# Kernel optimization log

Measured on AMD Instinct MI355X. Metric: run time of the kernel, lower is better.

Reference implementation:

```python
import jax, jax.numpy as jnp
import numpy as np

# Config mirrors init_kwargs
D_IN, D_OUT, HEADS, SEQ, BATCH = 1024, 64, 16, 2048, 2


def setup_inputs() -> dict:
    key = jax.random.key(0)
    kx, kq, kk, kv = jax.random.split(key, 4)
    scale = 1.0 / np.sqrt(D_IN)
    x = jax.random.normal(kx, (BATCH, SEQ, D_IN), dtype=jnp.float32)
    # Stacked per-head projection weights, [H, d_in, d_out] (qkv_bias=False)
    Wq = jax.random.normal(kq, (HEADS, D_IN, D_OUT), dtype=jnp.float32) * scale
    Wk = jax.random.normal(kk, (HEADS, D_IN, D_OUT), dtype=jnp.float32) * scale
    Wv = jax.random.normal(kv, (HEADS, D_IN, D_OUT), dtype=jnp.float32) * scale
    return {"x": x, "Wq": Wq, "Wk": Wk, "Wv": Wv}


def reference(x, Wq, Wk, Wv):
    # x: [B, S, d_in]; W*: [H, d_in, d_out]
    q = jnp.einsum("bsd,hde->bhse", x, Wq)
    k = jnp.einsum("bsd,hde->bhse", x, Wk)
    v = jnp.einsum("bsd,hde->bhse", x, Wv)
    scores = jnp.einsum("bhse,bhte->bhst", q, k) / jnp.sqrt(
        jnp.asarray(D_OUT, dtype=q.dtype)
    )
    S = x.shape[1]
    causal = jnp.tril(jnp.ones((S, S), dtype=bool))  # [S, S]
    scores = jnp.where(causal[None, None], scores, -jnp.inf)
    attn = jax.nn.softmax(scores, axis=-1)  # dropout=0.0 (eval)
    ctx = jnp.einsum("bhst,bhte->bhse", attn, v)  # [B, H, S, d_out]
    # concat heads on last dim -> [B, S, H*d_out]
    B, H, S2, E = ctx.shape
    return jnp.transpose(ctx, (0, 2, 1, 3)).reshape(B, S2, H * E)
```

## Files before the change

### kernel.cpp

```cpp
#include <hip/hip_runtime.h>
#include <hip/hip_bf16.h>
#include <math.h>

#define BATCH 2
#define SEQ   2048
#define DIN   1024
#define HEADS 16
#define EDIM  64

#define NX   (BATCH*SEQ*DIN)
#define NW   (3*HEADS*DIN*EDIM)
#define NQKV (BATCH*HEADS*SEQ*EDIM)

#define QSCALE 0.18033688011112042f

typedef __attribute__((ext_vector_type(8))) short short8;
typedef __attribute__((ext_vector_type(4))) float f32x4;

static __device__ __forceinline__ ushort f2bf(float f) {
    __hip_bfloat16 h = __float2bfloat16(f);
    return *reinterpret_cast<ushort*>(&h);
}

__global__ __launch_bounds__(256) void prep(
    const float* __restrict__ x, const float* __restrict__ Wq,
    const float* __restrict__ Wk, const float* __restrict__ Wv,
    ushort* __restrict__ xb, ushort* __restrict__ wt)
{
    const int t = threadIdx.x;
    if (blockIdx.x < 1024) {
        const int v0 = blockIdx.x * 256 + t;
#pragma unroll
        for (int i = 0; i < 4; ++i) {
            int i4 = (v0 + i * 262144) * 4;
            float4 f = *(const float4*)(x + i4);
            ushort4 o;
            o.x = f2bf(f.x); o.y = f2bf(f.y); o.z = f2bf(f.z); o.w = f2bf(f.w);
            *(ushort4*)(xb + i4) = o;
        }
    } else {
        const int bid = blockIdx.x - 1024;
        const int dt  = bid & 15;
        const int h   = (bid >> 4) & 15;
        const int mat = bid >> 8;

        const float* W = (mat == 0) ? Wq : (mat == 1) ? Wk : Wv;
        const float* src = W + ((size_t)h * DIN + dt * 64) * EDIM;
        ushort* dst = wt + ((size_t)(mat * HEADS + h) * EDIM) * DIN + dt * 64;

        __shared__ ushort T[64][68];
#pragma unroll
        for (int i = 0; i < 16; ++i) {
            int v = t + i * 256;
            int d = v >> 6, e = v & 63;
            T[d][e] = f2bf(src[(size_t)d * EDIM + e]);
        }
        __syncthreads();
#pragma unroll
        for (int i = 0; i < 4; ++i) {
            int v = t + i * 256;
            int e = v >> 4, d4 = (v & 15) << 2;
            ushort4 ov;
            ov.x = T[d4 + 0][e]; ov.y = T[d4 + 1][e];
            ov.z = T[d4 + 2][e]; ov.w = T[d4 + 3][e];
            *(ushort4*)&dst[(size_t)e * DIN + d4] = ov;
        }
    }
}

__global__ __launch_bounds__(256) void qkv_gemm(
    const ushort* __restrict__ xb, const ushort* __restrict__ wt,
    ushort* __restrict__ qkv)
{
    const int bid = blockIdx.x;
    const int xcd = bid & 7;
    const int idx = bid >> 3;
    const int mt  = (xcd >> 1) * 8 + idx / 12;
    const int nt  = (xcd & 1) * 12 + idx % 12;
    const int m0 = mt * 128, n0 = nt * 128;
    const int b  = mt >> 4;

    __shared__ ushort Xs[128][72];
    __shared__ ushort Ws[128][72];

    const int t    = threadIdx.x;
    const int lane = t & 63;
    const int w    = t >> 6;
    const int wr   = w >> 1, wc = w & 1;
    const int fr   = lane & 15;
    const int fk   = (lane >> 4) * 8;
    const int rg   = (lane >> 4) * 4;

    const ushort* xbase = xb + (size_t)m0 * DIN;
    const ushort* wbase = wt + (size_t)n0 * DIN;

    ushort4 xr[8], wr2[8];
#pragma unroll
    for (int i = 0; i < 8; ++i) {
        int v = t + i * 256;
        xr[i]  = *(const ushort4*)&xbase[(size_t)(v >> 4) * DIN + ((v & 15) << 2)];
        wr2[i] = *(const ushort4*)&wbase[(size_t)(v >> 4) * DIN + ((v & 15) << 2)];
    }

    f32x4 acc[4][4];
#pragma unroll
    for (int i = 0; i < 4; ++i)
#pragma unroll
        for (int j = 0; j < 4; ++j) acc[i][j] = (f32x4)0.f;

    for (int kt = 0; kt < DIN / 64; ++kt) {
        __syncthreads();
#pragma unroll
        for (int i = 0; i < 8; ++i) {
            int v = t + i * 256;
            *(ushort4*)&Xs[v >> 4][(v & 15) << 2] = xr[i];
            *(ushort4*)&Ws[v >> 4][(v & 15) << 2] = wr2[i];
        }
        __syncthreads();
        if (kt + 1 < DIN / 64) {
            const int k0 = (kt + 1) * 64;
#pragma unroll
            for (int i = 0; i < 8; ++i) {
                int v = t + i * 256;
                xr[i]  = *(const ushort4*)&xbase[(size_t)(v >> 4) * DIN + k0 + ((v & 15) << 2)];
                wr2[i] = *(const ushort4*)&wbase[(size_t)(v >> 4) * DIN + k0 + ((v & 15) << 2)];
            }
        }
        short8 a[4][2], bfr[4][2];
#pragma unroll
        for (int rb = 0; rb < 4; ++rb)
#pragma unroll
            for (int kk = 0; kk < 2; ++kk) {
                a[rb][kk]   = *(const short8*)&Xs[wr * 64 + rb * 16 + fr][kk * 32 + fk];
                bfr[rb][kk] = *(const short8*)&Ws[wc * 64 + rb * 16 + fr][kk * 32 + fk];
            }
#pragma unroll
        for (int kk = 0; kk < 2; ++kk)
#pragma unroll
            for (int rb = 0; rb < 4; ++rb)
#pragma unroll
                for (int cf = 0; cf < 4; ++cf)
                    acc[rb][cf] = __builtin_amdgcn_mfma_f32_16x16x32_bf16(a[rb][kk], bfr[cf][kk], acc[rb][cf], 0, 0, 0);
    }

    const int hg  = nt * 2 + wc;
    const int mat = hg >> 4;
    const int h   = hg & 15;
    const int s0  = (m0 & 2047) + wr * 64;
    if (mat < 2) {
        const float sc = (mat == 0) ? QSCALE : 1.0f;
        ushort* dst = qkv + (size_t)mat * NQKV
                    + ((size_t)((b * HEADS + h) * SEQ) + s0) * EDIM;
#pragma unroll
        for (int rb = 0; rb < 4; ++rb)
#pragma unroll
            for (int cf = 0; cf < 4; ++cf)
#pragma unroll
                for (int i = 0; i < 4; ++i)
                    dst[(size_t)(rb * 16 + rg + i) * EDIM + cf * 16 + fr] = f2bf(acc[rb][cf][i] * sc);
    } else {
        ushort* vtb = qkv + (size_t)2 * NQKV + ((size_t)(b * HEADS + h) * EDIM) * SEQ;
#pragma unroll
        for (int rb = 0; rb < 4; ++rb)
#pragma unroll
            for (int cf = 0; cf < 4; ++cf) {
                ushort4 ov;
                ov.x = f2bf(acc[rb][cf][0]); ov.y = f2bf(acc[rb][cf][1]);
                ov.z = f2bf(acc[rb][cf][2]); ov.w = f2bf(acc[rb][cf][3]);
                *(ushort4*)&vtb[(size_t)(cf * 16 + fr) * SEQ + s0 + rb * 16 + rg] = ov;
            }
    }
}

__global__ __launch_bounds__(512) void flash_mfma(
    const ushort* __restrict__ q, const ushort* __restrict__ k,
    const ushort* __restrict__ vt, float* __restrict__ out)
{
    const int bid = blockIdx.x;
    const int it  = 15 - (bid >> 5);
    const int bh  = bid & 31;
    const int b   = bh >> 4;
    const int h   = bh & 15;
    const int KT  = 2 * it + 2;

    const ushort* Qb  = q  + ((size_t)((b * HEADS + h) * SEQ) + it * 128) * EDIM;
    const ushort* Kb  = k  + ((size_t)((b * HEADS + h) * SEQ)) * EDIM;
    const ushort* Vtb = vt + ((size_t)((b * HEADS + h) * EDIM)) * SEQ;

    __shared__ ushort Ks_[2][64][72];
    __shared__ ushort Vs_[2][64][72];
    __shared__ ushort Ps_[8][16][72];

    const int t    = threadIdx.x;
    const int lane = t & 63;
    const int w    = t >> 6;
    const int fr   = lane & 15;
    const int fk   = (lane >> 4) * 8;
    const int rg   = (lane >> 4) * 4;

    const int srow = t >> 3;
    const int scol = (t & 7) * 8;

    const int wrow0 = it * 128 + w * 16;
    const int lastT = wrow0 >> 6;
    const int qrow  = wrow0 + fr;

    short8 qf[2];
#pragma unroll
    for (int kk = 0; kk < 2; ++kk)
        qf[kk] = *(const short8*)&Qb[(size_t)(w * 16 + fr) * EDIM + kk * 32 + fk];

    f32x4 o_[4];
#pragma unroll
    for (int cf = 0; cf < 4; ++cf) o_[cf] = (f32x4)0.f;
    float lpart = 0.f;

    uint4 krv = *(const uint4*)&Kb[(size_t)srow * EDIM + scol];
    uint4 vrv = *(const uint4*)&Vtb[(size_t)srow * SEQ + scol];
    *(uint4*)&Ks_[0][srow][scol] = krv;
    *(uint4*)&Vs_[0][srow][scol] = vrv;
    __syncthreads();

    for (int kt = 0; kt < KT; ++kt) {
        const int cur = kt & 1;

        if (kt + 1 < KT) {
            krv = *(const uint4*)&Kb[(size_t)((kt + 1) * 64 + srow) * EDIM + scol];
            vrv = *(const uint4*)&Vtb[(size_t)srow * SEQ + (kt + 1) * 64 + scol];
        }

        if (kt <= lastT) {
            f32x4 s[4];
#pragma unroll
            for (int cf = 0; cf < 4; ++cf) s[cf] = (f32x4)0.f;
#pragma unroll
            for (int cf = 0; cf < 4; ++cf)
#pragma unroll
                for (int kk = 0; kk < 2; ++kk) {
                    short8 kf = *(const short8*)&Ks_[cur][cf * 16 + fr][kk * 32 + fk];
                    s[cf] = __builtin_amdgcn_mfma_f32_16x16x32_bf16(kf, qf[kk], s[cf], 0, 0, 0);
                }

            const bool dm = (kt == lastT);
            if (dm) {
#pragma unroll
                for (int cf = 0; cf < 4; ++cf)
#pragma unroll
                    for (int i = 0; i < 4; ++i) {
                        int kpos = kt * 64 + cf * 16 + rg + i;
                        if (kpos > qrow) s[cf][i] = -1e30f;
                    }
            }

            float ls = 0.f;
#pragma unroll
            for (int cf = 0; cf < 4; ++cf) {
                float p0 = __builtin_amdgcn_exp2f(s[cf][0]);
                float p1 = __builtin_amdgcn_exp2f(s[cf][1]);
                float p2 = __builtin_amdgcn_exp2f(s[cf][2]);
                float p3 = __builtin_amdgcn_exp2f(s[cf][3]);
                ls += (p0 + p1) + (p2 + p3);
                uint2 pk;
                pk.x = (uint)f2bf(p0) | ((uint)f2bf(p1) << 16);
                pk.y = (uint)f2bf(p2) | ((uint)f2bf(p3) << 16);
                *(uint2*)&Ps_[w][fr][cf * 16 + rg] = pk;
            }
            lpart += ls;

            short8 pf[2];
#pragma unroll
            for (int kb = 0; kb < 2; ++kb)
                pf[kb] = *(const short8*)&Ps_[w][fr][kb * 32 + fk];
#pragma unroll
            for (int cf = 0; cf < 4; ++cf)
#pragma unroll
                for (int kb = 0; kb < 2; ++kb) {
                    short8 vf = *(const short8*)&Vs_[cur][cf * 16 + fr][kb * 32 + fk];
                    o_[cf] = __builtin_amdgcn_mfma_f32_16x16x32_bf16(vf, pf[kb], o_[cf], 0, 0, 0);
                }
        }

        if (kt + 1 < KT) {
            const int nxt = cur ^ 1;
            *(uint4*)&Ks_[nxt][srow][scol] = krv;
            *(uint4*)&Vs_[nxt][srow][scol] = vrv;
            __syncthreads();
        }
    }

    float ls = lpart;
    ls += __shfl_xor(ls, 16);
    ls += __shfl_xor(ls, 32);
    const float inv = 1.f / ls;

    float* rowp = out + ((size_t)(b * SEQ + qrow)) * (HEADS * EDIM) + h * EDIM;
#pragma unroll
    for (int cf = 0; cf < 4; ++cf) {
        f32x4 ov = o_[cf] * inv;
        *(f32x4*)&rowp[cf * 16 + rg] = ov;
    }
}

extern "C" void kernel_launch(void* const* d_in, const int* in_sizes, int n_in,
                              void* d_out, int out_size, void* d_ws, size_t ws_size,
                              hipStream_t stream) {
    const float* x  = (const float*)d_in[0];
    const float* Wq = (const float*)d_in[1];
    const float* Wk = (const float*)d_in[2];
    const float* Wv = (const float*)d_in[3];
    float* out = (float*)d_out;

    ushort* xb  = (ushort*)d_ws;
    ushort* wt  = xb + NX;
    ushort* qkv = wt + NW;

    prep<<<1792, 256, 0, stream>>>(x, Wq, Wk, Wv, xb, wt);
    qkv_gemm<<<768, 256, 0, stream>>>(xb, wt, qkv);
    flash_mfma<<<BATCH * HEADS * (SEQ / 128), 512, 0, stream>>>(
        qkv, qkv + NQKV, qkv + (size_t)2 * NQKV, out);
}
```

Baseline: 95.37 us.

## Give each flash wave two query row blocks and widen GEMM tile loads

The attention kernel drops from 8 waves of 16 query rows each to 4 waves of 32 rows each. Each K and V fragment read from shared memory is now reused for two MFMA row blocks, which halves LDS fragment traffic per unit of math but raises register pressure and cuts the number of waves per block. The QKV GEMM switches its global and LDS tile loads from 8-byte to 16-byte vectors, issuing half as many load and store instructions. The coarser causal work split means a wave may compute one extra partially masked tile.

```diff
diff --git a/kernel.cpp b/kernel.cpp
--- a/kernel.cpp
+++ b/kernel.cpp
@@ -94,12 +94,12 @@
     const ushort* xbase = xb + (size_t)m0 * DIN;
     const ushort* wbase = wt + (size_t)n0 * DIN;
 
-    ushort4 xr[8], wr2[8];
-#pragma unroll
-    for (int i = 0; i < 8; ++i) {
-        int v = t + i * 256;
-        xr[i]  = *(const ushort4*)&xbase[(size_t)(v >> 4) * DIN + ((v & 15) << 2)];
-        wr2[i] = *(const ushort4*)&wbase[(size_t)(v >> 4) * DIN + ((v & 15) << 2)];
+    uint4 xr[4], wr2[4];
+#pragma unroll
+    for (int i = 0; i < 4; ++i) {
+        int c = t + i * 256;
+        xr[i]  = *(const uint4*)&xbase[(size_t)(c >> 3) * DIN + ((c & 7) << 3)];
+        wr2[i] = *(const uint4*)&wbase[(size_t)(c >> 3) * DIN + ((c & 7) << 3)];
     }
 
     f32x4 acc[4][4];
@@ -111,19 +111,19 @@
     for (int kt = 0; kt < DIN / 64; ++kt) {
         __syncthreads();
 #pragma unroll
-        for (int i = 0; i < 8; ++i) {
-            int v = t + i * 256;
-            *(ushort4*)&Xs[v >> 4][(v & 15) << 2] = xr[i];
-            *(ushort4*)&Ws[v >> 4][(v & 15) << 2] = wr2[i];
+        for (int i = 0; i < 4; ++i) {
+            int c = t + i * 256;
+            *(uint4*)&Xs[c >> 3][(c & 7) << 3] = xr[i];
+            *(uint4*)&Ws[c >> 3][(c & 7) << 3] = wr2[i];
         }
         __syncthreads();
         if (kt + 1 < DIN / 64) {
             const int k0 = (kt + 1) * 64;
 #pragma unroll
-            for (int i = 0; i < 8; ++i) {
-                int v = t + i * 256;
-                xr[i]  = *(const ushort4*)&xbase[(size_t)(v >> 4) * DIN + k0 + ((v & 15) << 2)];
-                wr2[i] = *(const ushort4*)&wbase[(size_t)(v >> 4) * DIN + k0 + ((v & 15) << 2)];
+            for (int i = 0; i < 4; ++i) {
+                int c = t + i * 256;
+                xr[i]  = *(const uint4*)&xbase[(size_t)(c >> 3) * DIN + k0 + ((c & 7) << 3)];
+                wr2[i] = *(const uint4*)&wbase[(size_t)(c >> 3) * DIN + k0 + ((c & 7) << 3)];
             }
         }
         short8 a[4][2], bfr[4][2];
@@ -172,7 +172,7 @@
     }
 }
 
-__global__ __launch_bounds__(512) void flash_mfma(
+__global__ __launch_bounds__(256) void flash_mfma(
     const ushort* __restrict__ q, const ushort* __restrict__ k,
     const ushort* __restrict__ vt, float* __restrict__ out)
 {
@@ -189,7 +189,7 @@
 
     __shared__ ushort Ks_[2][64][72];
     __shared__ ushort Vs_[2][64][72];
-    __shared__ ushort Ps_[8][16][72];
+    __shared__ ushort Ps_[4][32][72];
 
     const int t    = threadIdx.x;
     const int lane = t & 63;
@@ -201,103 +201,142 @@
     const int srow = t >> 3;
     const int scol = (t & 7) * 8;
 
-    const int wrow0 = it * 128 + w * 16;
-    const int lastT = wrow0 >> 6;
-    const int qrow  = wrow0 + fr;
-
-    short8 qf[2];
-#pragma unroll
-    for (int kk = 0; kk < 2; ++kk)
-        qf[kk] = *(const short8*)&Qb[(size_t)(w * 16 + fr) * EDIM + kk * 32 + fk];
-
-    f32x4 o_[4];
-#pragma unroll
-    for (int cf = 0; cf < 4; ++cf) o_[cf] = (f32x4)0.f;
-    float lpart = 0.f;
-
-    uint4 krv = *(const uint4*)&Kb[(size_t)srow * EDIM + scol];
-    uint4 vrv = *(const uint4*)&Vtb[(size_t)srow * SEQ + scol];
-    *(uint4*)&Ks_[0][srow][scol] = krv;
-    *(uint4*)&Vs_[0][srow][scol] = vrv;
+    const int wrow0 = it * 128 + w * 32;
+    const int lastT = (wrow0 + 31) >> 6;
+    const int qrowA = wrow0 + fr;
+    const int qrowB = wrow0 + 16 + fr;
+
+    short8 qfA[2], qfB[2];
+#pragma unroll
+    for (int kk = 0; kk < 2; ++kk) {
+        qfA[kk] = *(const short8*)&Qb[(size_t)(w * 32 + fr) * EDIM + kk * 32 + fk];
+        qfB[kk] = *(const short8*)&Qb[(size_t)(w * 32 + 16 + fr) * EDIM + kk * 32 + fk];
+    }
+
+    f32x4 oA[4], oB[4];
+#pragma unroll
+    for (int cf = 0; cf < 4; ++cf) { oA[cf] = (f32x4)0.f; oB[cf] = (f32x4)0.f; }
+    float lpA = 0.f, lpB = 0.f;
+
+    uint4 krv[2], vrv[2];
+#pragma unroll
+    for (int i = 0; i < 2; ++i) {
+        int row = srow + i * 32;
+        krv[i] = *(const uint4*)&Kb[(size_t)row * EDIM + scol];
+        vrv[i] = *(const uint4*)&Vtb[(size_t)row * SEQ + scol];
+    }
+#pragma unroll
+    for (int i = 0; i < 2; ++i) {
+        int row = srow + i * 32;
+        *(uint4*)&Ks_[0][row][scol] = krv[i];
+        *(uint4*)&Vs_[0][row][scol] = vrv[i];
+    }
     __syncthreads();
 
     for (int kt = 0; kt < KT; ++kt) {
         const int cur = kt & 1;
 
         if (kt + 1 < KT) {
-            krv = *(const uint4*)&Kb[(size_t)((kt + 1) * 64 + srow) * EDIM + scol];
-            vrv = *(const uint4*)&Vtb[(size_t)srow * SEQ + (kt + 1) * 64 + scol];
+#pragma unroll
+            for (int i = 0; i < 2; ++i) {
+                int row = srow + i * 32;
+                krv[i] = *(const uint4*)&Kb[(size_t)((kt + 1) * 64 + row) * EDIM + scol];
+                vrv[i] = *(const uint4*)&Vtb[(size_t)row * SEQ + (kt + 1) * 64 + scol];
+            }
         }
 
         if (kt <= lastT) {
-            f32x4 s[4];
-#pragma unroll
-            for (int cf = 0; cf < 4; ++cf) s[cf] = (f32x4)0.f;
-#pragma unroll
-            for (int cf = 0; cf < 4; ++cf)
-#pragma unroll
-                for (int kk = 0; kk < 2; ++kk) {
-                    short8 kf = *(const short8*)&Ks_[cur][cf * 16 + fr][kk * 32 + fk];
-                    s[cf] = __builtin_amdgcn_mfma_f32_16x16x32_bf16(kf, qf[kk], s[cf], 0, 0, 0);
-                }
-
-            const bool dm = (kt == lastT);
-            if (dm) {
+            f32x4 sA[4], sB[4];
+#pragma unroll
+            for (int cf = 0; cf < 4; ++cf) { sA[cf] = (f32x4)0.f; sB[cf] = (f32x4)0.f; }
+#pragma unroll
+            for (int cf = 0; cf < 4; ++cf) {
+                short8 kf0 = *(const short8*)&Ks_[cur][cf * 16 + fr][fk];
+                short8 kf1 = *(const short8*)&Ks_[cur][cf * 16 + fr][32 + fk];
+                sA[cf] = __builtin_amdgcn_mfma_f32_16x16x32_bf16(kf0, qfA[0], sA[cf], 0, 0, 0);
+                sA[cf] = __builtin_amdgcn_mfma_f32_16x16x32_bf16(kf1, qfA[1], sA[cf], 0, 0, 0);
+                sB[cf] = __builtin_amdgcn_mfma_f32_16x16x32_bf16(kf0, qfB[0], sB[cf], 0, 0, 0);
+                sB[cf] = __builtin_amdgcn_mfma_f32_16x16x32_bf16(kf1, qfB[1], sB[cf], 0, 0, 0);
+            }
+
+            if (kt == lastT) {
 #pragma unroll
                 for (int cf = 0; cf < 4; ++cf)
 #pragma unroll
                     for (int i = 0; i < 4; ++i) {
                         int kpos = kt * 64 + cf * 16 + rg + i;
-                        if (kpos > qrow) s[cf][i] = -1e30f;
+                        if (kpos > qrowA) sA[cf][i] = -1e30f;
+                        if (kpos > qrowB) sB[cf][i] = -1e30f;
                     }
             }
 
-            float ls = 0.f;
+            float lsA = 0.f, lsB = 0.f;
 #pragma unroll
             for (int cf = 0; cf < 4; ++cf) {
-                float p0 = __builtin_amdgcn_exp2f(s[cf][0]);
-                float p1 = __builtin_amdgcn_exp2f(s[cf][1]);
-                float p2 = __builtin_amdgcn_exp2f(s[cf][2]);
-                float p3 = __builtin_amdgcn_exp2f(s[cf][3]);
-                ls += (p0 + p1) + (p2 + p3);
-                uint2 pk;
-                pk.x = (uint)f2bf(p0) | ((uint)f2bf(p1) << 16);
-                pk.y = (uint)f2bf(p2) | ((uint)f2bf(p3) << 16);
-                *(uint2*)&Ps_[w][fr][cf * 16 + rg] = pk;
-            }
-            lpart += ls;
-
-            short8 pf[2];
-#pragma unroll
-            for (int kb = 0; kb < 2; ++kb)
-                pf[kb] = *(const short8*)&Ps_[w][fr][kb * 32 + fk];
-#pragma unroll
-            for (int cf = 0; cf < 4; ++cf)
-#pragma unroll
-                for (int kb = 0; kb < 2; ++kb) {
-                    short8 vf = *(const short8*)&Vs_[cur][cf * 16 + fr][kb * 32 + fk];
-                    o_[cf] = __builtin_amdgcn_mfma_f32_16x16x32_bf16(vf, pf[kb], o_[cf], 0, 0, 0);
-                }
+                float a0 = __builtin_amdgcn_exp2f(sA[cf][0]);
+                float a1 = __builtin_amdgcn_exp2f(sA[cf][1]);
+                float a2 = __builtin_amdgcn_exp2f(sA[cf][2]);
+                float a3 = __builtin_amdgcn_exp2f(sA[cf][3]);
+                lsA += (a0 + a1) + (a2 + a3);
+                uint2 pka;
+                pka.x = (uint)f2bf(a0) | ((uint)f2bf(a1) << 16);
+                pka.y = (uint)f2bf(a2) | ((uint)f2bf(a3) << 16);
+                *(uint2*)&Ps_[w][fr][cf * 16 + rg] = pka;
+                float b0 = __builtin_amdgcn_exp2f(sB[cf][0]);
+                float b1 = __builtin_amdgcn_exp2f(sB[cf][1]);
+                float b2 = __builtin_amdgcn_exp2f(sB[cf][2]);
+                float b3 = __builtin_amdgcn_exp2f(sB[cf][3]);
+                lsB += (b0 + b1) + (b2 + b3);
+                uint2 pkb;
+                pkb.x = (uint)f2bf(b0) | ((uint)f2bf(b1) << 16);
+                pkb.y = (uint)f2bf(b2) | ((uint)f2bf(b3) << 16);
+                *(uint2*)&Ps_[w][16 + fr][cf * 16 + rg] = pkb;
+            }
+            lpA += lsA;
+            lpB += lsB;
+
+            short8 pfA0 = *(const short8*)&Ps_[w][fr][fk];
+            short8 pfA1 = *(const short8*)&Ps_[w][fr][32 + fk];
+            short8 pfB0 = *(const short8*)&Ps_[w][16 + fr][fk];
+            short8 pfB1 = *(const short8*)&Ps_[w][16 + fr][32 + fk];
+#pragma unroll
+            for (int cf = 0; cf < 4; ++cf) {
+                short8 vf0 = *(const short8*)&Vs_[cur][cf * 16 + fr][fk];
+                short8 vf1 = *(const short8*)&Vs_[cur][cf * 16 + fr][32 + fk];
+                oA[cf] = __builtin_amdgcn_mfma_f32_16x16x32_bf16(vf0, pfA0, oA[cf], 0, 0, 0);
+                oA[cf] = __builtin_amdgcn_mfma_f32_16x16x32_bf16(vf1, pfA1, oA[cf], 0, 0, 0);
+                oB[cf] = __builtin_amdgcn_mfma_f32_16x16x32_bf16(vf0, pfB0, oB[cf], 0, 0, 0);
+                oB[cf] = __builtin_amdgcn_mfma_f32_16x16x32_bf16(vf1, pfB1, oB[cf], 0, 0, 0);
+            }
         }
 
         if (kt + 1 < KT) {
             const int nxt = cur ^ 1;
-            *(uint4*)&Ks_[nxt][srow][scol] = krv;
-            *(uint4*)&Vs_[nxt][srow][scol] = vrv;
+#pragma unroll
+            for (int i = 0; i < 2; ++i) {
+                int row = srow + i * 32;
+                *(uint4*)&Ks_[nxt][row][scol] = krv[i];
+                *(uint4*)&Vs_[nxt][row][scol] = vrv[i];
+            }
             __syncthreads();
         }
     }
 
-    float ls = lpart;
-    ls += __shfl_xor(ls, 16);
-    ls += __shfl_xor(ls, 32);
-    const float inv = 1.f / ls;
-
-    float* rowp = out + ((size_t)(b * SEQ + qrow)) * (HEADS * EDIM) + h * EDIM;
+    float lA = lpA;
+    lA += __shfl_xor(lA, 16);
+    lA += __shfl_xor(lA, 32);
+    const float invA = 1.f / lA;
+    float lB = lpB;
+    lB += __shfl_xor(lB, 16);
+    lB += __shfl_xor(lB, 32);
+    const float invB = 1.f / lB;
+
+    float* rowpA = out + ((size_t)(b * SEQ + qrowA)) * (HEADS * EDIM) + h * EDIM;
+    float* rowpB = out + ((size_t)(b * SEQ + qrowB)) * (HEADS * EDIM) + h * EDIM;
 #pragma unroll
     for (int cf = 0; cf < 4; ++cf) {
-        f32x4 ov = o_[cf] * inv;
-        *(f32x4*)&rowp[cf * 16 + rg] = ov;
+        *(f32x4*)&rowpA[cf * 16 + rg] = oA[cf] * invA;
+        *(f32x4*)&rowpB[cf * 16 + rg] = oB[cf] * invB;
     }
 }
 
@@ -316,6 +355,6 @@
 
     prep<<<1792, 256, 0, stream>>>(x, Wq, Wk, Wv, xb, wt);
     qkv_gemm<<<768, 256, 0, stream>>>(xb, wt, qkv);
-    flash_mfma<<<BATCH * HEADS * (SEQ / 128), 512, 0, stream>>>(
+    flash_mfma<<<BATCH * HEADS * (SEQ / 128), 256, 0, stream>>>(
         qkv, qkv + NQKV, qkv + (size_t)2 * NQKV, out);
 }
```

Result: slower. 188.4 us (+97.5%).
